# Kernel optimization log

Hardware: AMD Instinct MI355X
Metric: run time of the kernel (lower is better)

Reference implementation:

```python
import jax, jax.numpy as jnp
import numpy as np

K_SIZE = 3
STRIDE = 1
DIL = 1
PAD = (K_SIZE - 1) // 2 * DIL          # padding of the deformable conv
OFF_PAD = (K_SIZE - 1) // 2            # padding of the offset conv
KK = K_SIZE * K_SIZE


def setup_inputs() -> dict:
    key = jax.random.key(0)
    k1, k2, k3, k4 = jax.random.split(key, 4)
    B, C, H, W = 4, 256, 64, 64
    O = 256
    x = jax.random.normal(k1, (B, C, H, W), jnp.float32)
    # offset/mask conv params (small so sampled offsets stay in a realistic range)
    w_off = jax.random.normal(k2, (3 * KK, C, K_SIZE, K_SIZE), jnp.float32) * 0.01
    b_off = jax.random.normal(k3, (3 * KK,), jnp.float32) * 0.01
    # deformable conv weight (conv_dcn has bias=False in the source)
    w_dcn = jax.random.normal(k4, (O, C, K_SIZE, K_SIZE), jnp.float32) * (1.0 / np.sqrt(C * KK))
    return {"x": x, "w_off": w_off, "b_off": b_off, "w_dcn": w_dcn}


def _bilinear_sample(x, ys, xs):
    """x: [B,C,H,W]; ys, xs: [B,KK,Ho,Wo] fractional coords. Zero outside bounds.
    Returns [B,C,KK,Ho,Wo]."""
    B, C, H, W = x.shape
    _, K, Ho, Wo = ys.shape
    y0 = jnp.floor(ys)
    x0 = jnp.floor(xs)
    y1, x1 = y0 + 1.0, x0 + 1.0
    wy1 = ys - y0
    wy0 = 1.0 - wy1
    wx1 = xs - x0
    wx0 = 1.0 - wx1
    x_flat = x.reshape(B, C, H * W)

    def gather_term(yi, xi, wt):
        valid = (yi >= 0) & (yi < H) & (xi >= 0) & (xi < W)
        yc = jnp.clip(yi, 0, H - 1).astype(jnp.int32)
        xc = jnp.clip(xi, 0, W - 1).astype(jnp.int32)
        idx = (yc * W + xc).reshape(B, -1)                      # [B, K*Ho*Wo]
        g = jax.vmap(lambda xf, i: xf[:, i])(x_flat, idx)       # [B, C, K*Ho*Wo]
        w = (wt * valid.astype(wt.dtype)).reshape(B, 1, -1)
        return g * w

    out = (gather_term(y0, x0, wy0 * wx0)
           + gather_term(y0, x1, wy0 * wx1)
           + gather_term(y1, x0, wy1 * wx0)
           + gather_term(y1, x1, wy1 * wx1))
    return out.reshape(B, C, K, Ho, Wo)


def _dcn_v2(x, w_off, b_off, w_dcn):
    B, C, H, W = x.shape
    # offset/mask conv (standard conv, padding (k-1)//2)
    om = jax.lax.conv_general_dilated(
        x, w_off, (STRIDE, STRIDE), [(OFF_PAD, OFF_PAD)] * 2,
        dimension_numbers=("NCHW", "OIHW", "NCHW")) + b_off[None, :, None, None]
    offset = om[:, :2 * KK]                 # [B, 2*KK, Ho, Wo] as (dy0,dx0,dy1,dx1,...)
    mask = jax.nn.sigmoid(om[:, 2 * KK:])   # [B, KK, Ho, Wo]
    Ho, Wo = offset.shape[2], offset.shape[3]

    off = offset.reshape(B, KK, 2, Ho, Wo)
    off_y, off_x = off[:, :, 0], off[:, :, 1]

    kh = (jnp.arange(KK) // K_SIZE).astype(jnp.float32)
    kw = (jnp.arange(KK) % K_SIZE).astype(jnp.float32)
    py = (jnp.arange(Ho) * STRIDE - PAD).astype(jnp.float32)
    px = (jnp.arange(Wo) * STRIDE - PAD).astype(jnp.float32)

    ys = py[None, None, :, None] + (kh * DIL)[None, :, None, None] + off_y
    xs = px[None, None, None, :] + (kw * DIL)[None, :, None, None] + off_x

    sampled = _bilinear_sample(x, ys, xs)           # [B,C,KK,Ho,Wo]
    sampled = sampled * mask[:, None]               # modulated (DCNv2)
    w = w_dcn.reshape(w_dcn.shape[0], C, KK)
    return jnp.einsum("bckhw,ock->bohw", sampled, w)


def reference(x, w_off, b_off, w_dcn):
    return _dcn_v2(x, w_off, b_off, w_dcn)
```

## Files before the change

### kernel.cpp

```cpp
#include <hip/hip_runtime.h>

typedef __attribute__((ext_vector_type(8))) short short8;
typedef __attribute__((ext_vector_type(4))) float f32x4;

#define CIN 256
#define OUTC 256
#define HWW 4096
#define IMG_H 64
#define IMG_W 64
#define SROW 264
#define SB __builtin_amdgcn_sched_barrier(0)
#define GLOAD(dst, addr) \
    asm volatile("global_load_dwordx4 %0, %1, off" : "=v"(dst) : "v"(addr) : "memory")
#define WAITVM(n) asm volatile("s_waitcnt vmcnt(" #n ")" ::: "memory")
#define WAITLGKM  asm volatile("s_waitcnt lgkmcnt(0)" ::: "memory")

__device__ __forceinline__ short f2bf(float f) {
    unsigned u = __float_as_uint(f);
    u += 0x7fffu + ((u >> 16) & 1u);
    return (short)(u >> 16);
}
__device__ __forceinline__ float bf2f(short s) {
    return __uint_as_float(((unsigned)(unsigned short)s) << 16);
}

__global__ __launch_bounds__(256) void prep(const float* __restrict__ x,
                                            const float* __restrict__ w_dcn,
                                            const float* __restrict__ w_off,
                                            short* __restrict__ xT,
                                            short* __restrict__ wF,
                                            short* __restrict__ wFo) {
    int bid = blockIdx.x;
    if (bid < 1024) {
        __shared__ float T[64][65];
        int p0 = (bid & 63) * 64;
        int c0 = ((bid >> 6) & 3) * 64;
        int b  = bid >> 8;
        int j = threadIdx.x & 63, i = threadIdx.x >> 6;
        const float* xb = x + ((size_t)b * CIN + c0) * HWW + p0;
#pragma unroll
        for (int k = 0; k < 16; ++k) {
            int row = i * 16 + k;
            T[row][j] = xb[(size_t)row * HWW + j];
        }
        __syncthreads();
        short* xTb = xT + ((size_t)b * HWW + p0) * CIN + c0;
#pragma unroll
        for (int k = 0; k < 16; ++k) {
            int prow = i * 16 + k;
            xTb[(size_t)prow * CIN + j] = f2bf(T[j][prow]);
        }
    } else if (bid < 1312) {
        int g = (bid - 1024) * 256 + threadIdx.x;
        int lane = g & 63;
        int rest = g >> 6;
        int octile = rest & 15;
        int step = rest >> 4;
        int kp = step >> 3, chv = step & 7;
        int oc = octile * 16 + (lane & 15);
        int cbase = chv * 32 + (lane >> 4) * 8;
        short8 v;
#pragma unroll
        for (int j = 0; j < 8; ++j)
            v[j] = f2bf(w_dcn[oc * 2304 + (cbase + j) * 9 + kp]);
        *(short8*)(wF + (size_t)g * 8) = v;
    } else {
        int g = (bid - 1312) * 256 + threadIdx.x;
        int lane = g & 63;
        int rest = g >> 6;
        int octile = rest & 1;
        int step = rest >> 1;
        int kp = step >> 3, chv = step & 7;
        int oc = octile * 16 + (lane & 15);
        int cbase = chv * 32 + (lane >> 4) * 8;
        short8 v;
#pragma unroll
        for (int j = 0; j < 8; ++j)
            v[j] = (oc < 27) ? f2bf(w_off[(oc * 256 + cbase + j) * 9 + kp]) : (short)0;
        *(short8*)(wFo + (size_t)g * 8) = v;
    }
}

__global__ __launch_bounds__(256) void offs_mfma(
        const short* __restrict__ xT, const short* __restrict__ wFo,
        float* __restrict__ P) {
    __shared__ short Sm[2][32 * SROW];

    int tid = threadIdx.x;
    int d = blockIdx.x;
    int L = (d & 7) * 64 + (d >> 3);
    int b = L >> 7;
    int ph = L & 127;
    int pbase = ph * 32;
    int prow = ph >> 1;
    int pc0 = (ph & 1) * 32;
    const short* xTb = xT + (size_t)b * HWW * CIN;

    int lane = tid & 63, wave = tid >> 6;
    int fr = lane & 15, fq = lane >> 4;
    int octile = wave & 1, pxt = wave >> 1;

    short8 st[4];

    auto loads = [&](int kp) {
        int yy = prow - 1 + kp / 3;
        int dx = kp % 3 - 1;
#pragma unroll
        for (int it = 0; it < 4; ++it) {
            int item = tid + it * 256;
            int cg8 = item & 31, px = item >> 5;
            int xx = pc0 + px + dx;
            bool ok = (yy >= 0 && yy < IMG_H && xx >= 0 && xx < IMG_W);
            int idx = ok ? ((yy * IMG_W + xx) * CIN + cg8 * 8) : 0;
            short8 v = *(const short8*)&xTb[idx];
            if (!ok) v = (short8){0,0,0,0,0,0,0,0};
            st[it] = v;
        }
    };
    auto writes = [&](int bufi) {
#pragma unroll
        for (int it = 0; it < 4; ++it) {
            int item = tid + it * 256;
            int cg8 = item & 31, px = item >> 5;
            *(short8*)&Sm[bufi][px * SROW + cg8 * 8] = st[it];
        }
    };

    f32x4 acc = (f32x4){0.f, 0.f, 0.f, 0.f};

    loads(0); writes(0);
    __syncthreads();
    for (int kp = 0; kp < 9; ++kp) {
        short8 aF[8];
#pragma unroll
        for (int chv = 0; chv < 8; ++chv)
            aF[chv] = *(const short8*)(wFo +
                    (((size_t)((kp * 8 + chv) * 2 + octile)) * 64 + lane) * 8);
        if (kp < 8) loads(kp + 1);
        const short* SmB = Sm[kp & 1];
#pragma unroll
        for (int chv = 0; chv < 8; ++chv) {
            short8 bF = *(const short8*)&SmB[(pxt * 16 + fr) * SROW + chv * 32 + fq * 8];
            acc = __builtin_amdgcn_mfma_f32_16x16x32_bf16(aF[chv], bF, acc, 0, 0, 0);
        }
        if (kp < 8) writes((kp + 1) & 1);
        __syncthreads();
    }

#pragma unroll
    for (int r = 0; r < 4; ++r) {
        int oc = octile * 16 + fq * 4 + r;
        if (oc < 27)
            P[((size_t)b * 32 + oc) * HWW + pbase + pxt * 16 + fr] = acc[r];
    }
}

__global__ __launch_bounds__(512, 2) void dcn_main(
        const short* __restrict__ xT, const float* __restrict__ b_off,
        const float* __restrict__ P, const short* __restrict__ wF,
        float* __restrict__ out) {
    __shared__ short Sm[2][32 * 64 * 8];
    __shared__ float4 preW[576];
    __shared__ int4  preI[576];

    int tid = threadIdx.x;
    int d = blockIdx.x;
    int L = (d & 7) * 32 + (d >> 3);
    int b = L >> 6;
    int row = L & 63;
    int pbase = row * 64;
    const short* xTb = xT + (size_t)b * HWW * CIN;

    for (int e = tid; e < 576; e += 512) {
        int px = e & 63, kp = e >> 6;
        int p = pbase + px;
        float oy = P[((size_t)b * 32 + 2 * kp) * HWW + p] + b_off[2 * kp];
        float ox = P[((size_t)b * 32 + 2 * kp + 1) * HWW + p] + b_off[2 * kp + 1];
        float ml = P[((size_t)b * 32 + 18 + kp) * HWW + p] + b_off[18 + kp];
        float m = 1.0f / (1.0f + expf(-ml));
        float ys = (float)(row - 1 + kp / 3) + oy;
        float xs = (float)(px - 1 + kp % 3) + ox;
        float y0f = floorf(ys), x0f = floorf(xs);
        float fy = ys - y0f, fx = xs - x0f;
        int iy0 = (int)y0f, ix0 = (int)x0f;
        int iy1 = iy0 + 1, ix1 = ix0 + 1;
        float vy0 = (iy0 >= 0 && iy0 < IMG_H) ? 1.f : 0.f;
        float vy1 = (iy1 >= 0 && iy1 < IMG_H) ? 1.f : 0.f;
        float vx0 = (ix0 >= 0 && ix0 < IMG_W) ? 1.f : 0.f;
        float vx1 = (ix1 >= 0 && ix1 < IMG_W) ? 1.f : 0.f;
        int ry0 = min(max(iy0, 0), IMG_H - 1) * IMG_W;
        int ry1 = min(max(iy1, 0), IMG_H - 1) * IMG_W;
        int cx0 = min(max(ix0, 0), IMG_W - 1);
        int cx1 = min(max(ix1, 0), IMG_W - 1);
        float wy0 = 1.f - fy, wy1 = fy, wx0 = 1.f - fx, wx1 = fx;
        preW[e] = make_float4(wy0 * wx0 * vy0 * vx0 * m, wy0 * wx1 * vy0 * vx1 * m,
                              wy1 * wx0 * vy1 * vx0 * m, wy1 * wx1 * vy1 * vx1 * m);
        preI[e] = make_int4((ry0 + cx0) * CIN, (ry0 + cx1) * CIN,
                            (ry1 + cx0) * CIN, (ry1 + cx1) * CIN);
    }
    __syncthreads();

    int lane = tid & 63, wave = tid >> 6;
    int fr = lane & 15, fq = lane >> 4;
    int chunk = tid & 31, p0 = tid >> 5;
    int co = chunk * 8;

    auto soff = [](int s, int px) { return (s * 64 + (px & 32) + ((px & 31) ^ s)) * 8; };

    short8 stO[4][4];
    short8 aFc[16];

    auto issue_taps = [&](int kq) {
#pragma unroll
        for (int it = 0; it < 4; ++it) {
            int px = p0 + it * 16;
            int4 iv = preI[kq * 64 + px];
            GLOAD(stO[it][0], (const short8*)&xTb[iv.x + co]);
            GLOAD(stO[it][1], (const short8*)&xTb[iv.y + co]);
            GLOAD(stO[it][2], (const short8*)&xTb[iv.z + co]);
            GLOAD(stO[it][3], (const short8*)&xTb[iv.w + co]);
        }
    };
    auto combine_writes = [&](int kq, int bufi) {
#pragma unroll
        for (int it = 0; it < 4; ++it) {
            int px = p0 + it * 16;
            float4 wv = preW[kq * 64 + px];
            short8 o;
#pragma unroll
            for (int j = 0; j < 8; ++j) {
                float v = wv.x * bf2f(stO[it][0][j]) + wv.y * bf2f(stO[it][1][j]) +
                          wv.z * bf2f(stO[it][2][j]) + wv.w * bf2f(stO[it][3][j]);
                o[j] = f2bf(v);
            }
            *(short8*)&Sm[bufi][soff(chunk, px)] = o;
        }
    };

    f32x4 acc[2][4];
#pragma unroll
    for (int m = 0; m < 2; ++m)
#pragma unroll
        for (int n = 0; n < 4; ++n)
            acc[m][n] = (f32x4){0.f, 0.f, 0.f, 0.f};

    issue_taps(0);
    SB;

#pragma unroll
    for (int kp = 0; kp < 9; ++kp) {
        const int bufi = kp & 1;
#pragma unroll
        for (int chv = 0; chv < 8; ++chv)
#pragma unroll
            for (int m = 0; m < 2; ++m)
                GLOAD(aFc[chv * 2 + m], (const short8*)(wF +
                        (((size_t)((kp * 8 + chv) * 16 + wave * 2 + m)) * 64 + lane) * 8));
        SB;
        WAITVM(16); SB;
        combine_writes(kp, bufi);
        SB;
        if (kp < 8) issue_taps(kp + 1);
        SB;
        WAITLGKM;
        __builtin_amdgcn_s_barrier();
        SB;
        if (kp < 8) { WAITVM(16); } else { WAITVM(0); }
        SB;
        {
            const short* SmB = Sm[bufi];
#pragma unroll
            for (int chv = 0; chv < 8; ++chv)
#pragma unroll
                for (int n = 0; n < 4; ++n) {
                    short8 bF = *(const short8*)&SmB[soff(chv * 4 + fq, n * 16 + fr)];
#pragma unroll
                    for (int m = 0; m < 2; ++m)
                        acc[m][n] = __builtin_amdgcn_mfma_f32_16x16x32_bf16(
                                aFc[chv * 2 + m], bF, acc[m][n], 0, 0, 0);
                }
        }
        SB;
    }

    float* outb = out + (size_t)b * (OUTC * HWW) + pbase;
#pragma unroll
    for (int m = 0; m < 2; ++m)
#pragma unroll
        for (int n = 0; n < 4; ++n)
#pragma unroll
            for (int r = 0; r < 4; ++r)
                outb[(size_t)(wave * 32 + m * 16 + fq * 4 + r) * HWW + n * 16 + fr] =
                        acc[m][n][r];
}

extern "C" void kernel_launch(void* const* d_in, const int* in_sizes, int n_in,
                              void* d_out, int out_size, void* d_ws, size_t ws_size,
                              hipStream_t stream) {
    const float* x     = (const float*)d_in[0];
    const float* w_off = (const float*)d_in[1];
    const float* b_off = (const float*)d_in[2];
    const float* w_dcn = (const float*)d_in[3];
    float* out = (float*)d_out;

    short* xT  = (short*)d_ws;
    float* P   = (float*)(xT + (size_t)4 * HWW * CIN);
    short* wF  = (short*)(P + (size_t)4 * 32 * HWW);
    short* wFo = wF + (size_t)73728 * 8;

    prep<<<1348, 256, 0, stream>>>(x, w_dcn, w_off, xT, wF, wFo);
    offs_mfma<<<512, 256, 0, stream>>>(xT, wFo, P);
    dcn_main<<<256, 512, 0, stream>>>(xT, b_off, P, wF, out);
}
```

Before: 58.54 us.

## Split each tap into two channel halves and double-buffer weights and taps

The main loop now runs over 18 steps, each covering one kernel tap and half the input channels. The sampled-tap gathers and the weight fragments for the next step are issued one step ahead into double-buffered registers, and the shared staging buffer is halved. The aim is deeper overlap of global loads with MFMA work and lower LDS use, which could raise occupancy. In exchange it adds more barriers per output and changes the LDS swizzle pattern.

```diff
diff --git a/kernel.cpp b/kernel.cpp
--- a/kernel.cpp
+++ b/kernel.cpp
@@ -159,7 +159,7 @@
         const short* __restrict__ xT, const float* __restrict__ b_off,
         const float* __restrict__ P, const short* __restrict__ wF,
         float* __restrict__ out) {
-    __shared__ short Sm[2][32 * 64 * 8];
+    __shared__ short Sm[2][16 * 64 * 8];
     __shared__ float4 preW[576];
     __shared__ int4  preI[576];
 
@@ -202,38 +202,48 @@
 
     int lane = tid & 63, wave = tid >> 6;
     int fr = lane & 15, fq = lane >> 4;
-    int chunk = tid & 31, p0 = tid >> 5;
-    int co = chunk * 8;
-
-    auto soff = [](int s, int px) { return (s * 64 + (px & 32) + ((px & 31) ^ s)) * 8; };
-
-    short8 stO[4][4];
-    short8 aFc[16];
-
-    auto issue_taps = [&](int kq) {
-#pragma unroll
-        for (int it = 0; it < 4; ++it) {
-            int px = p0 + it * 16;
-            int4 iv = preI[kq * 64 + px];
-            GLOAD(stO[it][0], (const short8*)&xTb[iv.x + co]);
-            GLOAD(stO[it][1], (const short8*)&xTb[iv.y + co]);
-            GLOAD(stO[it][2], (const short8*)&xTb[iv.z + co]);
-            GLOAD(stO[it][3], (const short8*)&xTb[iv.w + co]);
+    int chunk = tid & 15, p0 = tid >> 4;
+
+    auto soff = [](int s, int px) { return (s * 64 + (px & 48) + ((px & 15) ^ s)) * 8; };
+
+    short8 stO[2][8];
+    short8 aFd[2][8];
+
+    auto issue = [&](int t, int par) {
+        int kp = t >> 1, ks = t & 1;
+        int co = ks * 128 + chunk * 8;
+#pragma unroll
+        for (int cl = 0; cl < 4; ++cl)
+#pragma unroll
+            for (int m = 0; m < 2; ++m)
+                GLOAD(aFd[par][cl * 2 + m], (const short8*)(wF +
+                        (((size_t)((kp * 8 + ks * 4 + cl) * 16 + wave * 2 + m)) * 64 + lane) * 8));
+#pragma unroll
+        for (int it = 0; it < 2; ++it) {
+            int px = p0 + it * 32;
+            int4 iv = preI[kp * 64 + px];
+            GLOAD(stO[par][it * 4 + 0], (const short8*)&xTb[iv.x + co]);
+            GLOAD(stO[par][it * 4 + 1], (const short8*)&xTb[iv.y + co]);
+            GLOAD(stO[par][it * 4 + 2], (const short8*)&xTb[iv.z + co]);
+            GLOAD(stO[par][it * 4 + 3], (const short8*)&xTb[iv.w + co]);
         }
     };
-    auto combine_writes = [&](int kq, int bufi) {
-#pragma unroll
-        for (int it = 0; it < 4; ++it) {
-            int px = p0 + it * 16;
-            float4 wv = preW[kq * 64 + px];
+    auto combine = [&](int t, int par) {
+        int kp = t >> 1;
+#pragma unroll
+        for (int it = 0; it < 2; ++it) {
+            int px = p0 + it * 32;
+            float4 wv = preW[kp * 64 + px];
             short8 o;
 #pragma unroll
             for (int j = 0; j < 8; ++j) {
-                float v = wv.x * bf2f(stO[it][0][j]) + wv.y * bf2f(stO[it][1][j]) +
-                          wv.z * bf2f(stO[it][2][j]) + wv.w * bf2f(stO[it][3][j]);
+                float v = wv.x * bf2f(stO[par][it * 4 + 0][j]) +
+                          wv.y * bf2f(stO[par][it * 4 + 1][j]) +
+                          wv.z * bf2f(stO[par][it * 4 + 2][j]) +
+                          wv.w * bf2f(stO[par][it * 4 + 3][j]);
                 o[j] = f2bf(v);
             }
-            *(short8*)&Sm[bufi][soff(chunk, px)] = o;
+            *(short8*)&Sm[par][soff(chunk, px)] = o;
         }
     };
 
@@ -244,40 +254,32 @@
         for (int n = 0; n < 4; ++n)
             acc[m][n] = (f32x4){0.f, 0.f, 0.f, 0.f};
 
-    issue_taps(0);
+    issue(0, 0);
     SB;
 
 #pragma unroll
-    for (int kp = 0; kp < 9; ++kp) {
-        const int bufi = kp & 1;
-#pragma unroll
-        for (int chv = 0; chv < 8; ++chv)
-#pragma unroll
-            for (int m = 0; m < 2; ++m)
-                GLOAD(aFc[chv * 2 + m], (const short8*)(wF +
-                        (((size_t)((kp * 8 + chv) * 16 + wave * 2 + m)) * 64 + lane) * 8));
-        SB;
-        WAITVM(16); SB;
-        combine_writes(kp, bufi);
-        SB;
-        if (kp < 8) issue_taps(kp + 1);
+    for (int t = 0; t < 18; ++t) {
+        const int par = t & 1;
+        if (t < 17) issue(t + 1, par ^ 1);
+        SB;
+        if (t < 17) { WAITVM(16); } else { WAITVM(0); }
+        SB;
+        combine(t, par);
         SB;
         WAITLGKM;
         __builtin_amdgcn_s_barrier();
         SB;
-        if (kp < 8) { WAITVM(16); } else { WAITVM(0); }
-        SB;
         {
-            const short* SmB = Sm[bufi];
-#pragma unroll
-            for (int chv = 0; chv < 8; ++chv)
+            const short* SmB = Sm[par];
+#pragma unroll
+            for (int cl = 0; cl < 4; ++cl)
 #pragma unroll
                 for (int n = 0; n < 4; ++n) {
-                    short8 bF = *(const short8*)&SmB[soff(chv * 4 + fq, n * 16 + fr)];
+                    short8 bF = *(const short8*)&SmB[soff(cl * 4 + fq, n * 16 + fr)];
 #pragma unroll
                     for (int m = 0; m < 2; ++m)
                         acc[m][n] = __builtin_amdgcn_mfma_f32_16x16x32_bf16(
-                                aFc[chv * 2 + m], bF, acc[m][n], 0, 0, 0);
+                                aFd[par][cl * 2 + m], bF, acc[m][n], 0, 0, 0);
                 }
         }
         SB;
```

After: 60.99 us. 4.2% more time.

## Restructure DCN main loop into 24 channel-by-tap steps with register double buffering

Applied to the files above, without the earlier changes.

Reorders the reduction in the main kernel from 9 kernel-point steps over all 256 channels to 24 steps, each covering 32 channels and 3 kernel points. Tap gathers become 8-byte loads and weights are reordered to channel-major to match. Both tap data and weight fragments are double-buffered in registers so the next step's loads are in flight during the current combine and MFMA work. This is meant to shrink LDS use and hide gather latency, at the cost of more loop iterations, an extra barrier per step and smaller, less efficient global loads.

```diff
diff --git a/kernel.cpp b/kernel.cpp
--- a/kernel.cpp
+++ b/kernel.cpp
@@ -1,6 +1,7 @@
 #include <hip/hip_runtime.h>
 
 typedef __attribute__((ext_vector_type(8))) short short8;
+typedef __attribute__((ext_vector_type(4))) short short4v;
 typedef __attribute__((ext_vector_type(4))) float f32x4;
 
 #define CIN 256
@@ -10,7 +11,9 @@
 #define IMG_W 64
 #define SROW 264
 #define SB __builtin_amdgcn_sched_barrier(0)
-#define GLOAD(dst, addr) \
+#define GLOAD2(dst, addr) \
+    asm volatile("global_load_dwordx2 %0, %1, off" : "=v"(dst) : "v"(addr) : "memory")
+#define GLOAD4(dst, addr) \
     asm volatile("global_load_dwordx4 %0, %1, off" : "=v"(dst) : "v"(addr) : "memory")
 #define WAITVM(n) asm volatile("s_waitcnt vmcnt(" #n ")" ::: "memory")
 #define WAITLGKM  asm volatile("s_waitcnt lgkmcnt(0)" ::: "memory")
@@ -56,9 +59,9 @@
         int rest = g >> 6;
         int octile = rest & 15;
         int step = rest >> 4;
-        int kp = step >> 3, chv = step & 7;
+        int ch = step / 9, kp = step % 9;
         int oc = octile * 16 + (lane & 15);
-        int cbase = chv * 32 + (lane >> 4) * 8;
+        int cbase = ch * 32 + (lane >> 4) * 8;
         short8 v;
 #pragma unroll
         for (int j = 0; j < 8; ++j)
@@ -155,11 +158,12 @@
     }
 }
 
+#define SMR 104
 __global__ __launch_bounds__(512, 2) void dcn_main(
         const short* __restrict__ xT, const float* __restrict__ b_off,
         const float* __restrict__ P, const short* __restrict__ wF,
         float* __restrict__ out) {
-    __shared__ short Sm[2][32 * 64 * 8];
+    __shared__ short Sm[2][64 * SMR];
     __shared__ float4 preW[576];
     __shared__ int4  preI[576];
 
@@ -202,38 +206,45 @@
 
     int lane = tid & 63, wave = tid >> 6;
     int fr = lane & 15, fq = lane >> 4;
-    int chunk = tid & 31, p0 = tid >> 5;
-    int co = chunk * 8;
-
-    auto soff = [](int s, int px) { return (s * 64 + (px & 32) + ((px & 31) ^ s)) * 8; };
-
-    short8 stO[4][4];
-    short8 aFc[16];
-
-    auto issue_taps = [&](int kq) {
-#pragma unroll
-        for (int it = 0; it < 4; ++it) {
-            int px = p0 + it * 16;
-            int4 iv = preI[kq * 64 + px];
-            GLOAD(stO[it][0], (const short8*)&xTb[iv.x + co]);
-            GLOAD(stO[it][1], (const short8*)&xTb[iv.y + co]);
-            GLOAD(stO[it][2], (const short8*)&xTb[iv.z + co]);
-            GLOAD(stO[it][3], (const short8*)&xTb[iv.w + co]);
+    int jh = tid & 1;
+    int chunk = (tid >> 1) & 3;
+    int spx = tid >> 3;
+    int cbase = chunk * 8 + jh * 4;
+
+    short4v stA[12], stB[12];
+    short8  aA[6],  aB[6];
+
+    auto issue = [&](int t, short4v* st, short8* aF) {
+        int ch = t / 3, r = t % 3;
+        int co = ch * 32 + cbase;
+#pragma unroll
+        for (int i = 0; i < 3; ++i) {
+            int kp = r * 3 + i;
+#pragma unroll
+            for (int m = 0; m < 2; ++m)
+                GLOAD4(aF[i * 2 + m], (const short8*)(wF +
+                        (((size_t)((ch * 9 + kp) * 16 + wave * 2 + m)) * 64 + lane) * 8));
+            int4 iv = preI[kp * 64 + spx];
+            GLOAD2(st[i * 4 + 0], (const short4v*)&xTb[iv.x + co]);
+            GLOAD2(st[i * 4 + 1], (const short4v*)&xTb[iv.y + co]);
+            GLOAD2(st[i * 4 + 2], (const short4v*)&xTb[iv.z + co]);
+            GLOAD2(st[i * 4 + 3], (const short4v*)&xTb[iv.w + co]);
         }
     };
-    auto combine_writes = [&](int kq, int bufi) {
-#pragma unroll
-        for (int it = 0; it < 4; ++it) {
-            int px = p0 + it * 16;
-            float4 wv = preW[kq * 64 + px];
-            short8 o;
-#pragma unroll
-            for (int j = 0; j < 8; ++j) {
-                float v = wv.x * bf2f(stO[it][0][j]) + wv.y * bf2f(stO[it][1][j]) +
-                          wv.z * bf2f(stO[it][2][j]) + wv.w * bf2f(stO[it][3][j]);
-                o[j] = f2bf(v);
+    auto combine = [&](int t, short4v* st, int bufi) {
+        int r = t % 3;
+#pragma unroll
+        for (int i = 0; i < 3; ++i) {
+            int kp = r * 3 + i;
+            float4 wv = preW[kp * 64 + spx];
+            short4v o;
+#pragma unroll
+            for (int e = 0; e < 4; ++e) {
+                float v = wv.x * bf2f(st[i * 4 + 0][e]) + wv.y * bf2f(st[i * 4 + 1][e]) +
+                          wv.z * bf2f(st[i * 4 + 2][e]) + wv.w * bf2f(st[i * 4 + 3][e]);
+                o[e] = f2bf(v);
             }
-            *(short8*)&Sm[bufi][soff(chunk, px)] = o;
+            *(short4v*)&Sm[bufi][spx * SMR + i * 32 + cbase] = o;
         }
     };
 
@@ -244,42 +255,38 @@
         for (int n = 0; n < 4; ++n)
             acc[m][n] = (f32x4){0.f, 0.f, 0.f, 0.f};
 
-    issue_taps(0);
+    issue(0, stA, aA);
     SB;
 
 #pragma unroll
-    for (int kp = 0; kp < 9; ++kp) {
-        const int bufi = kp & 1;
-#pragma unroll
-        for (int chv = 0; chv < 8; ++chv)
-#pragma unroll
-            for (int m = 0; m < 2; ++m)
-                GLOAD(aFc[chv * 2 + m], (const short8*)(wF +
-                        (((size_t)((kp * 8 + chv) * 16 + wave * 2 + m)) * 64 + lane) * 8));
-        SB;
-        WAITVM(16); SB;
-        combine_writes(kp, bufi);
-        SB;
-        if (kp < 8) issue_taps(kp + 1);
-        SB;
+    for (int t = 0; t < 24; ++t) {
+        short4v* stC = (t & 1) ? stB : stA;
+        short8*  aC  = (t & 1) ? aB  : aA;
+        short4v* stN = (t & 1) ? stA : stB;
+        short8*  aN  = (t & 1) ? aA  : aB;
+        if (t < 23) issue(t + 1, stN, aN);
+        SB;
+        if (t < 23) { WAITVM(18); } else { WAITVM(0); }
+        SB;
+        combine(t, stC, t & 1);
         WAITLGKM;
         __builtin_amdgcn_s_barrier();
         SB;
-        if (kp < 8) { WAITVM(16); } else { WAITVM(0); }
-        SB;
         {
-            const short* SmB = Sm[bufi];
-#pragma unroll
-            for (int chv = 0; chv < 8; ++chv)
+            const short* SmB = Sm[t & 1];
+#pragma unroll
+            for (int i = 0; i < 3; ++i)
 #pragma unroll
                 for (int n = 0; n < 4; ++n) {
-                    short8 bF = *(const short8*)&SmB[soff(chv * 4 + fq, n * 16 + fr)];
+                    short8 bF = *(const short8*)&SmB[(n * 16 + fr) * SMR + i * 32 + fq * 8];
 #pragma unroll
                     for (int m = 0; m < 2; ++m)
                         acc[m][n] = __builtin_amdgcn_mfma_f32_16x16x32_bf16(
-                                aFc[chv * 2 + m], bF, acc[m][n], 0, 0, 0);
+                                aC[i * 2 + m], bF, acc[m][n], 0, 0, 0);
                 }
         }
+        SB;
+        __builtin_amdgcn_s_barrier();
         SB;
     }
 
```

Result: slower. 71.74 us (+22.5%).

## Split dcn_main into half-row blocks with finer-grained 64-channel pipelined stages

Applied to the files above, without the earlier changes.

Each block of dcn_main now covers half an image row (32 pixels) with 256 threads, and the grid grows to 512 blocks. The tap-by-tap loop becomes 36 stages of 64 input channels each, which double-buffers both the weight fragments and the gathered samples in registers and shrinks shared memory use. The goal is more blocks in flight and finer overlap of the gather loads with the MFMA work. In exchange each weight fragment is loaded twice as often across blocks (one load per half-row), and there are four times as many barriers.

```diff
diff --git a/kernel.cpp b/kernel.cpp
--- a/kernel.cpp
+++ b/kernel.cpp
@@ -10,7 +10,7 @@
 #define IMG_W 64
 #define SROW 264
 #define SB __builtin_amdgcn_sched_barrier(0)
-#define GLOAD(dst, addr) \
+#define GLOAD4(dst, addr) \
     asm volatile("global_load_dwordx4 %0, %1, off" : "=v"(dst) : "v"(addr) : "memory")
 #define WAITVM(n) asm volatile("s_waitcnt vmcnt(" #n ")" ::: "memory")
 #define WAITLGKM  asm volatile("s_waitcnt lgkmcnt(0)" ::: "memory")
@@ -155,31 +155,34 @@
     }
 }
 
-__global__ __launch_bounds__(512, 2) void dcn_main(
+__global__ __launch_bounds__(256, 2) void dcn_main(
         const short* __restrict__ xT, const float* __restrict__ b_off,
         const float* __restrict__ P, const short* __restrict__ wF,
         float* __restrict__ out) {
-    __shared__ short Sm[2][32 * 64 * 8];
-    __shared__ float4 preW[576];
-    __shared__ int4  preI[576];
+    __shared__ short Sm[2][32 * 72];
+    __shared__ float4 preW[288];
+    __shared__ int4  preI[288];
 
     int tid = threadIdx.x;
     int d = blockIdx.x;
-    int L = (d & 7) * 32 + (d >> 3);
+    int half = d >> 8;
+    int d2 = d & 255;
+    int L = (d2 & 7) * 32 + (d2 >> 3);
     int b = L >> 6;
     int row = L & 63;
-    int pbase = row * 64;
+    int pc0 = half * 32;
+    int pbase = row * 64 + pc0;
     const short* xTb = xT + (size_t)b * HWW * CIN;
 
-    for (int e = tid; e < 576; e += 512) {
-        int px = e & 63, kp = e >> 6;
+    for (int e = tid; e < 288; e += 256) {
+        int px = e & 31, kp = e >> 5;
         int p = pbase + px;
         float oy = P[((size_t)b * 32 + 2 * kp) * HWW + p] + b_off[2 * kp];
         float ox = P[((size_t)b * 32 + 2 * kp + 1) * HWW + p] + b_off[2 * kp + 1];
         float ml = P[((size_t)b * 32 + 18 + kp) * HWW + p] + b_off[18 + kp];
         float m = 1.0f / (1.0f + expf(-ml));
         float ys = (float)(row - 1 + kp / 3) + oy;
-        float xs = (float)(px - 1 + kp % 3) + ox;
+        float xs = (float)(pc0 + px - 1 + kp % 3) + ox;
         float y0f = floorf(ys), x0f = floorf(xs);
         float fy = ys - y0f, fx = xs - x0f;
         int iy0 = (int)y0f, ix0 = (int)x0f;
@@ -202,95 +205,97 @@
 
     int lane = tid & 63, wave = tid >> 6;
     int fr = lane & 15, fq = lane >> 4;
-    int chunk = tid & 31, p0 = tid >> 5;
-    int co = chunk * 8;
-
-    auto soff = [](int s, int px) { return (s * 64 + (px & 32) + ((px & 31) ^ s)) * 8; };
-
-    short8 stO[4][4];
-    short8 aFc[16];
-
-    auto issue_taps = [&](int kq) {
-#pragma unroll
-        for (int it = 0; it < 4; ++it) {
-            int px = p0 + it * 16;
-            int4 iv = preI[kq * 64 + px];
-            GLOAD(stO[it][0], (const short8*)&xTb[iv.x + co]);
-            GLOAD(stO[it][1], (const short8*)&xTb[iv.y + co]);
-            GLOAD(stO[it][2], (const short8*)&xTb[iv.z + co]);
-            GLOAD(stO[it][3], (const short8*)&xTb[iv.w + co]);
-        }
+    int spx = tid >> 3;
+    int chunk = tid & 7;
+
+    auto soff = [](int s, int px) { return px * 72 + ((s ^ (px & 7)) * 8); };
+
+    short8 stA[4], stB[4];
+    short8 aA[8],  aB[8];
+
+    auto issue = [&](int t, short8* aF, short8* st) {
+        int kp = t >> 2, q = t & 3;
+#pragma unroll
+        for (int chv2 = 0; chv2 < 2; ++chv2) {
+            int chv = q * 2 + chv2;
+#pragma unroll
+            for (int m = 0; m < 4; ++m)
+                GLOAD4(aF[chv2 * 4 + m], (const short8*)(wF +
+                        (((size_t)((kp * 8 + chv) * 16 + wave * 4 + m)) * 64 + lane) * 8));
+        }
+        int co = q * 64 + chunk * 8;
+        int4 iv = preI[kp * 32 + spx];
+        GLOAD4(st[0], (const short8*)&xTb[iv.x + co]);
+        GLOAD4(st[1], (const short8*)&xTb[iv.y + co]);
+        GLOAD4(st[2], (const short8*)&xTb[iv.z + co]);
+        GLOAD4(st[3], (const short8*)&xTb[iv.w + co]);
     };
-    auto combine_writes = [&](int kq, int bufi) {
-#pragma unroll
-        for (int it = 0; it < 4; ++it) {
-            int px = p0 + it * 16;
-            float4 wv = preW[kq * 64 + px];
-            short8 o;
-#pragma unroll
-            for (int j = 0; j < 8; ++j) {
-                float v = wv.x * bf2f(stO[it][0][j]) + wv.y * bf2f(stO[it][1][j]) +
-                          wv.z * bf2f(stO[it][2][j]) + wv.w * bf2f(stO[it][3][j]);
-                o[j] = f2bf(v);
+    auto combine = [&](int t, short8* st, int par) {
+        int kp = t >> 2;
+        float4 wv = preW[kp * 32 + spx];
+        short8 o;
+#pragma unroll
+        for (int j = 0; j < 8; ++j) {
+            float v = wv.x * bf2f(st[0][j]) + wv.y * bf2f(st[1][j]) +
+                      wv.z * bf2f(st[2][j]) + wv.w * bf2f(st[3][j]);
+            o[j] = f2bf(v);
+        }
+        *(short8*)&Sm[par][soff(chunk, spx)] = o;
+    };
+
+    f32x4 acc[4][2];
+#pragma unroll
+    for (int m = 0; m < 4; ++m)
+#pragma unroll
+        for (int n = 0; n < 2; ++n)
+            acc[m][n] = (f32x4){0.f, 0.f, 0.f, 0.f};
+
+    issue(0, aA, stA);
+    SB;
+
+    for (int kp = 0; kp < 9; ++kp) {
+#pragma unroll
+        for (int q = 0; q < 4; ++q) {
+            int t = kp * 4 + q;
+            int par = q & 1;
+            short8* aC = par ? aB : aA;
+            short8* sC = par ? stB : stA;
+            short8* aN = par ? aA : aB;
+            short8* sN = par ? stA : stB;
+            if (t < 35) issue(t + 1, aN, sN);
+            SB;
+            if (t < 35) { WAITVM(12); } else { WAITVM(0); }
+            SB;
+            combine(t, sC, par);
+            WAITLGKM;
+            __builtin_amdgcn_s_barrier();
+            SB;
+            {
+                const short* SmB = Sm[par];
+#pragma unroll
+                for (int chv2 = 0; chv2 < 2; ++chv2)
+#pragma unroll
+                    for (int n = 0; n < 2; ++n) {
+                        int px = n * 16 + fr;
+                        short8 bF = *(const short8*)&SmB[soff(chv2 * 4 + fq, px)];
+#pragma unroll
+                        for (int m = 0; m < 4; ++m)
+                            acc[m][n] = __builtin_amdgcn_mfma_f32_16x16x32_bf16(
+                                    aC[chv2 * 4 + m], bF, acc[m][n], 0, 0, 0);
+                    }
             }
-            *(short8*)&Sm[bufi][soff(chunk, px)] = o;
-        }
-    };
-
-    f32x4 acc[2][4];
-#pragma unroll
-    for (int m = 0; m < 2; ++m)
-#pragma unroll
-        for (int n = 0; n < 4; ++n)
-            acc[m][n] = (f32x4){0.f, 0.f, 0.f, 0.f};
-
-    issue_taps(0);
-    SB;
-
-#pragma unroll
-    for (int kp = 0; kp < 9; ++kp) {
-        const int bufi = kp & 1;
-#pragma unroll
-        for (int chv = 0; chv < 8; ++chv)
-#pragma unroll
-            for (int m = 0; m < 2; ++m)
-                GLOAD(aFc[chv * 2 + m], (const short8*)(wF +
-                        (((size_t)((kp * 8 + chv) * 16 + wave * 2 + m)) * 64 + lane) * 8));
-        SB;
-        WAITVM(16); SB;
-        combine_writes(kp, bufi);
-        SB;
-        if (kp < 8) issue_taps(kp + 1);
-        SB;
-        WAITLGKM;
-        __builtin_amdgcn_s_barrier();
-        SB;
-        if (kp < 8) { WAITVM(16); } else { WAITVM(0); }
-        SB;
-        {
-            const short* SmB = Sm[bufi];
-#pragma unroll
-            for (int chv = 0; chv < 8; ++chv)
-#pragma unroll
-                for (int n = 0; n < 4; ++n) {
-                    short8 bF = *(const short8*)&SmB[soff(chv * 4 + fq, n * 16 + fr)];
-#pragma unroll
-                    for (int m = 0; m < 2; ++m)
-                        acc[m][n] = __builtin_amdgcn_mfma_f32_16x16x32_bf16(
-                                aFc[chv * 2 + m], bF, acc[m][n], 0, 0, 0);
-                }
-        }
-        SB;
+            SB;
+        }
     }
 
     float* outb = out + (size_t)b * (OUTC * HWW) + pbase;
 #pragma unroll
-    for (int m = 0; m < 2; ++m)
-#pragma unroll
-        for (int n = 0; n < 4; ++n)
+    for (int m = 0; m < 4; ++m)
+#pragma unroll
+        for (int n = 0; n < 2; ++n)
 #pragma unroll
             for (int r = 0; r < 4; ++r)
-                outb[(size_t)(wave * 32 + m * 16 + fq * 4 + r) * HWW + n * 16 + fr] =
+                outb[(size_t)(wave * 64 + m * 16 + fq * 4 + r) * HWW + n * 16 + fr] =
                         acc[m][n][r];
 }
 
@@ -310,5 +315,5 @@
 
     prep<<<1348, 256, 0, stream>>>(x, w_dcn, w_off, xT, wF, wFo);
     offs_mfma<<<512, 256, 0, stream>>>(xT, wFo, P);
-    dcn_main<<<256, 512, 0, stream>>>(xT, b_off, P, wF, out);
-}
+    dcn_main<<<512, 256, 0, stream>>>(xT, b_off, P, wF, out);
+}
```

Measured after the change: 64.52 us. +10.2%, slower.
